# Performance work log

Hardware: AMD Instinct MI355X
Metric: run time of the kernel (lower is better)

The kernel has to match this reference:

```python
import jax, jax.numpy as jnp
import numpy as np

C, C_H, N_HEAD = 8, 1, 8
B, S, I = 1, 4096, 1024


def setup_inputs() -> dict:
    key = jax.random.key(0)
    ks = jax.random.split(key, 8)
    m = jax.random.normal(ks[0], (B, S, I, C), dtype=jnp.float32)
    mask = jnp.ones((B, S, I), dtype=jnp.float32)
    sc = 0.1
    return {
        "m": m,
        "mask": mask,
        "ln_gamma": jnp.ones((C,), jnp.float32),
        "ln_beta": jnp.zeros((C,), jnp.float32),
        "Wq": jax.random.normal(ks[1], (C, C_H * N_HEAD), jnp.float32) * sc,
        "Wk": jax.random.normal(ks[2], (C, C_H), jnp.float32) * sc,
        "Wv": jax.random.normal(ks[3], (C, C_H), jnp.float32) * sc,
        "Wg": jax.random.normal(ks[4], (C, C_H * N_HEAD), jnp.float32) * sc,
        "bg": jax.random.normal(ks[5], (C_H * N_HEAD,), jnp.float32) * sc,
        "Wo": jax.random.normal(ks[6], (C_H * N_HEAD, C), jnp.float32) * sc,
        "bo": jax.random.normal(ks[7], (C,), jnp.float32) * sc,
    }


def reference(m, mask, ln_gamma, ln_beta, Wq, Wk, Wv, Wg, bg, Wo, bo):
    # m: (B, s, i, c) -> work in (B, i, s, c); mask: (B, s, i) -> (B, i, s)
    mt = jnp.swapaxes(m, -2, -3)
    mk = jnp.swapaxes(mask, -1, -2)
    c_h = Wk.shape[1]
    h = Wq.shape[1] // c_h
    Bz, iz, sz, _ = mt.shape

    # LayerNorm over channel dim (eps=1e-5, population variance)
    mu = jnp.mean(mt, axis=-1, keepdims=True)
    var = jnp.mean(jnp.square(mt - mu), axis=-1, keepdims=True)
    mn = (mt - mu) / jnp.sqrt(var + 1e-5) * ln_gamma + ln_beta  # (B,i,s,c)

    # Masked mean pool over sequences -> global query per residue column
    q = jnp.sum(mn * mk[..., None], axis=-2) / (jnp.sum(mk, axis=-1)[..., None] + 1e-5)  # (B,i,c)

    q = (q @ Wq) * (c_h ** -0.5)          # (B,i,h*c_h)
    k = mn @ Wk                           # (B,i,s,c_h)  shared across heads
    v = mn @ Wv                           # (B,i,s,c_h)
    g = jax.nn.sigmoid(mn @ Wg + bg)      # (B,i,s,h*c_h)

    q = q.reshape(Bz, iz, h, c_h)
    g = g.reshape(Bz, iz, sz, h, c_h)

    bias = 1e9 * (mk - 1.0)               # (B,i,s)
    a = jnp.einsum('bihd,bisd->bihs', q, k) + bias[..., None, :]
    a = jax.nn.softmax(a, axis=-1)        # (B,i,h,s)
    o = jnp.einsum('bihs,bisd->bihd', a, v)  # (B,i,h,c_h)

    o = o[..., None, :, :] * g            # (B,i,s,h,c_h) gated, broadcast over s
    o = o.reshape(Bz, iz, sz, h * c_h) @ Wo + bo  # (B,i,s,c)
    return jnp.swapaxes(o, -2, -3)        # (B,s,i,c)
```

## Files before the change

### kernel.cpp

```cpp
#include <hip/hip_runtime.h>

#define I_LEN 1024
#define S_LEN 4096

typedef float f32x4 __attribute__((ext_vector_type(4)));

__device__ __forceinline__ unsigned int f2h(float f) {
  _Float16 h = (_Float16)f; unsigned short u;
  __builtin_memcpy(&u, &h, 2); return (unsigned int)u;
}
__device__ __forceinline__ float h2f(unsigned int u) {
  unsigned short s = (unsigned short)u; _Float16 h;
  __builtin_memcpy(&h, &s, 2); return (float)h;
}

__global__ __launch_bounds__(256, 2) void msa_k1a(
    const float* __restrict__ m, const float* __restrict__ mask,
    const float* __restrict__ lng, const float* __restrict__ lnb,
    const float* __restrict__ Wk, const float* __restrict__ Wv,
    unsigned int* __restrict__ kvS, float* __restrict__ qpart)
{
  const int b  = blockIdx.x;
  const int cg = b & 15;
  const int sb = b >> 4;
  const int t  = threadIdx.x;
  const int w  = t >> 6;
  const int l  = t & 63;
  const int i  = cg * 64 + w * 16 + (l & 15);
  const int sg = l >> 4;
  const int s0 = sb * 32 + sg * 8;

  float swk = 0.f, swv = 0.f, kb = 0.f, vb = 0.f;
#pragma unroll
  for (int c = 0; c < 8; ++c) {
    swk = fmaf(lng[c], Wk[c], swk);  swv = fmaf(lng[c], Wv[c], swv);
    kb  = fmaf(lnb[c], Wk[c], kb);   vb  = fmaf(lnb[c], Wv[c], vb);
  }

  float4 L[8], H[8]; float MK[8];
#pragma unroll
  for (int r = 0; r < 8; ++r) {
    const size_t base = (size_t)((s0 + r) * I_LEN + i);
    const float4* mp = (const float4*)(m + base * 8);
    L[r] = mp[0]; H[r] = mp[1];
    MK[r] = mask[base];
  }
  __builtin_amdgcn_sched_barrier(0);

  float qnx[8] = {0,0,0,0,0,0,0,0};
  float qd = 0.f;
#pragma unroll
  for (int r = 0; r < 8; ++r) {
    const size_t base = (size_t)((s0 + r) * I_LEN + i);
    float x[8] = {L[r].x, L[r].y, L[r].z, L[r].w, H[r].x, H[r].y, H[r].z, H[r].w};
    const float mk = MK[r];
    float su = 0.f, s2 = 0.f;
#pragma unroll
    for (int c = 0; c < 8; ++c) { su += x[c]; s2 = fmaf(x[c], x[c], s2); }
    const float mu   = su * 0.125f;
    const float var  = s2 * 0.125f - mu * mu;
    const float rstd = rsqrtf(var + 1e-5f);
    float dk = 0.f, dv = 0.f;
#pragma unroll
    for (int c = 0; c < 8; ++c) {
      const float xg = x[c] * lng[c];
      dk = fmaf(xg, Wk[c], dk);
      dv = fmaf(xg, Wv[c], dv);
      x[c] = xg;
    }
    const float kk = fmaf(rstd, fmaf(-mu, swk, dk), kb);
    const float vv = fmaf(rstd, fmaf(-mu, swv, dv), vb);
    kvS[base] = (mk > 0.5f) ? ((f2h(kk) << 16) | f2h(vv)) : 0xFFFFFFFFu;

    const float mr  = mk * rstd;
    const float mmr = -mu * mr;
#pragma unroll
    for (int c = 0; c < 8; ++c)
      qnx[c] = fmaf(x[c], mr, fmaf(lng[c], mmr, qnx[c]));
    qd += mk;
  }

  float red[9];
#pragma unroll
  for (int q = 0; q < 9; ++q) {
    float x = (q < 8) ? qnx[q] : qd;
    x += __shfl_xor(x, 16);
    x += __shfl_xor(x, 32);
    red[q] = x;
  }
  if (l < 16) {
    float4* pp = (float4*)(qpart + ((size_t)sb * I_LEN + i) * 12);
    pp[0] = make_float4(red[0], red[1], red[2], red[3]);
    pp[1] = make_float4(red[4], red[5], red[6], red[7]);
    pp[2] = make_float4(red[8], 0.f, 0.f, 0.f);
  }
}

__global__ __launch_bounds__(64) void msa_k1b(
    const float* __restrict__ lnb, const float* __restrict__ Wq,
    const float* __restrict__ qpart, float* __restrict__ qtab)
{
  const int l  = threadIdx.x;
  const int i  = blockIdx.x * 4 + (l & 3);
  const int sl = l >> 2;
  float acc[9] = {0,0,0,0,0,0,0,0,0};
#pragma unroll
  for (int it = 0; it < 8; ++it) {
    const int sb = sl + it * 16;
    const float4* p = (const float4*)(qpart + ((size_t)sb * I_LEN + i) * 12);
    const float4 a = p[0], b4 = p[1], c4 = p[2];
    acc[0] += a.x;  acc[1] += a.y;  acc[2] += a.z;  acc[3] += a.w;
    acc[4] += b4.x; acc[5] += b4.y; acc[6] += b4.z; acc[7] += b4.w;
    acc[8] += c4.x;
  }
#pragma unroll
  for (int q = 0; q < 9; ++q) {
    float x = acc[q];
    x += __shfl_xor(x, 4);
    x += __shfl_xor(x, 8);
    x += __shfl_xor(x, 16);
    x += __shfl_xor(x, 32);
    acc[q] = x;
  }
  if (l < 4) {
    const float d   = acc[8];
    const float inv = 1.0f / (d + 1e-5f);
    float qs[8];
#pragma unroll
    for (int c = 0; c < 8; ++c) qs[c] = (acc[c] + lnb[c] * d) * inv;
    float qv[8];
#pragma unroll
    for (int h = 0; h < 8; ++h) {
      float v = 0.f;
#pragma unroll
      for (int c = 0; c < 8; ++c) v = fmaf(qs[c], Wq[c * 8 + h], v);
      qv[h] = v;
    }
    float4* qp = (float4*)(qtab + (size_t)i * 8);
    qp[0] = make_float4(qv[0], qv[1], qv[2], qv[3]);
    qp[1] = make_float4(qv[4], qv[5], qv[6], qv[7]);
  }
}

__global__ __launch_bounds__(256, 2) void msa_k1c(
    const unsigned int* __restrict__ kvS, const float* __restrict__ qtab,
    float* __restrict__ spart)
{
  const int b  = blockIdx.x;
  const int cg = b & 15;
  const int sb = b >> 4;
  const int t  = threadIdx.x;
  const int w  = t >> 6;
  const int l  = t & 63;
  const int i  = cg * 64 + w * 16 + (l & 15);
  const int sg = l >> 4;
  const int s0 = sb * 32 + sg * 8;

  const float4* qp = (const float4*)(qtab + (size_t)i * 8);
  const float4 q0 = qp[0], q1 = qp[1];
  const float qh[8] = {q0.x, q0.y, q0.z, q0.w, q1.x, q1.y, q1.z, q1.w};

  unsigned int W[8];
#pragma unroll
  for (int r = 0; r < 8; ++r)
    W[r] = kvS[(size_t)((s0 + r) * I_LEN + i)];
  __builtin_amdgcn_sched_barrier(0);

  float se[8] = {0,0,0,0,0,0,0,0};
  float sv[8] = {0,0,0,0,0,0,0,0};
#pragma unroll
  for (int r = 0; r < 8; ++r) {
    const unsigned int wv = W[r];
    const bool on = (wv != 0xFFFFFFFFu);
    const float kk = h2f(wv >> 16);
    const float vv = on ? h2f(wv & 0xFFFFu) : 0.0f;
#pragma unroll
    for (int h = 0; h < 8; ++h) {
      const float e = on ? __expf(qh[h] * kk) : 0.0f;
      se[h] += e;
      sv[h] = fmaf(e, vv, sv[h]);
    }
  }
  float red[16];
#pragma unroll
  for (int q = 0; q < 16; ++q) {
    float x = (q < 8) ? se[q] : sv[q - 8];
    x += __shfl_xor(x, 16);
    x += __shfl_xor(x, 32);
    red[q] = x;
  }
  if (l < 16) {
    float4* pp = (float4*)(spart + ((size_t)sb * I_LEN + i) * 16);
    pp[0] = make_float4(red[0],  red[1],  red[2],  red[3]);
    pp[1] = make_float4(red[4],  red[5],  red[6],  red[7]);
    pp[2] = make_float4(red[8],  red[9],  red[10], red[11]);
    pp[3] = make_float4(red[12], red[13], red[14], red[15]);
  }
}

__global__ __launch_bounds__(64) void msa_k1d(
    const float* __restrict__ spart, float* __restrict__ o_tab)
{
  const int l  = threadIdx.x;
  const int i  = blockIdx.x * 4 + (l & 3);
  const int sl = l >> 2;
  float acc[16] = {0,0,0,0,0,0,0,0,0,0,0,0,0,0,0,0};
#pragma unroll
  for (int it = 0; it < 8; ++it) {
    const int sb = sl + it * 16;
    const float4* p = (const float4*)(spart + ((size_t)sb * I_LEN + i) * 16);
    const float4 a = p[0], b4 = p[1], c4 = p[2], d4 = p[3];
    acc[0]  += a.x;  acc[1]  += a.y;  acc[2]  += a.z;  acc[3]  += a.w;
    acc[4]  += b4.x; acc[5]  += b4.y; acc[6]  += b4.z; acc[7]  += b4.w;
    acc[8]  += c4.x; acc[9]  += c4.y; acc[10] += c4.z; acc[11] += c4.w;
    acc[12] += d4.x; acc[13] += d4.y; acc[14] += d4.z; acc[15] += d4.w;
  }
#pragma unroll
  for (int q = 0; q < 16; ++q) {
    float x = acc[q];
    x += __shfl_xor(x, 4);
    x += __shfl_xor(x, 8);
    x += __shfl_xor(x, 16);
    x += __shfl_xor(x, 32);
    acc[q] = x;
  }
  if (l < 4) {
    float4* op = (float4*)(o_tab + (size_t)i * 8);
    op[0] = make_float4(acc[8]  / acc[0], acc[9]  / acc[1],
                        acc[10] / acc[2], acc[11] / acc[3]);
    op[1] = make_float4(acc[12] / acc[4], acc[13] / acc[5],
                        acc[14] / acc[6], acc[15] / acc[7]);
  }
}

__global__ __launch_bounds__(256, 2) void msa_k2(
    const float* __restrict__ m,
    const float* __restrict__ lng, const float* __restrict__ lnb,
    const float* __restrict__ Wg, const float* __restrict__ bg,
    const float* __restrict__ Wo, const float* __restrict__ bo,
    const float* __restrict__ o_tab, float* __restrict__ out)
{
  const int tid = blockIdx.x * 256 + threadIdx.x;
  const int i = tid & (I_LEN - 1);

  float sgv[8], tbv[8];
#pragma unroll
  for (int h = 0; h < 8; ++h) {
    float s = 0.f, tb = bg[h];
#pragma unroll
    for (int c = 0; c < 8; ++c) {
      s  = fmaf(lng[c], Wg[c * 8 + h], s);
      tb = fmaf(lnb[c], Wg[c * 8 + h], tb);
    }
    sgv[h] = s; tbv[h] = tb;
  }

  const float4* op = (const float4*)(o_tab + (size_t)i * 8);
  const float4 o1 = op[0], o2 = op[1];
  const float A[8] = {o1.x, o1.y, o1.z, o1.w, o2.x, o2.y, o2.z, o2.w};

#pragma unroll
  for (int g2 = 0; g2 < 2; ++g2) {
    float4 LO[4], HI[4];
#pragma unroll
    for (int r = 0; r < 4; ++r) {
      const size_t p = (size_t)tid + (size_t)(g2 * 4 + r) * 524288;
      const float4* mp = (const float4*)(m + p * 8);
      LO[r] = mp[0]; HI[r] = mp[1];
    }
    __builtin_amdgcn_sched_barrier(0);
#pragma unroll
    for (int r = 0; r < 4; ++r) {
      const size_t p = (size_t)tid + (size_t)(g2 * 4 + r) * 524288;
      float x[8] = {LO[r].x, LO[r].y, LO[r].z, LO[r].w,
                    HI[r].x, HI[r].y, HI[r].z, HI[r].w};
      float su = 0.f, s2 = 0.f;
#pragma unroll
      for (int c = 0; c < 8; ++c) { su += x[c]; s2 = fmaf(x[c], x[c], s2); }
      const float mu   = su * 0.125f;
      const float var  = s2 * 0.125f - mu * mu;
      const float rstd = rsqrtf(var + 1e-5f);
#pragma unroll
      for (int c = 0; c < 8; ++c) x[c] *= lng[c];
      float acc[8];
#pragma unroll
      for (int c = 0; c < 8; ++c) acc[c] = bo[c];
#pragma unroll
      for (int h = 0; h < 8; ++h) {
        float d = 0.f;
#pragma unroll
        for (int c = 0; c < 8; ++c) d = fmaf(x[c], Wg[c * 8 + h], d);
        const float gl = fmaf(rstd, fmaf(-mu, sgv[h], d), tbv[h]);
        const float gv = A[h] / (1.0f + __expf(-gl));
#pragma unroll
        for (int c = 0; c < 8; ++c) acc[c] = fmaf(gv, Wo[h * 8 + c], acc[c]);
      }
      f32x4* outp = (f32x4*)(out + p * 8);
      f32x4 r0 = {acc[0], acc[1], acc[2], acc[3]};
      f32x4 r1 = {acc[4], acc[5], acc[6], acc[7]};
      __builtin_nontemporal_store(r0, outp);
      __builtin_nontemporal_store(r1, outp + 1);
    }
  }
}

extern "C" void kernel_launch(void* const* d_in, const int* in_sizes, int n_in,
                              void* d_out, int out_size, void* d_ws, size_t ws_size,
                              hipStream_t stream) {
  const float* m    = (const float*)d_in[0];
  const float* mask = (const float*)d_in[1];
  const float* lng  = (const float*)d_in[2];
  const float* lnb  = (const float*)d_in[3];
  const float* Wq   = (const float*)d_in[4];
  const float* Wk   = (const float*)d_in[5];
  const float* Wv   = (const float*)d_in[6];
  const float* Wg   = (const float*)d_in[7];
  const float* bg   = (const float*)d_in[8];
  const float* Wo   = (const float*)d_in[9];
  const float* bo   = (const float*)d_in[10];
  float* out = (float*)d_out;

  char* ws = (char*)d_ws;
  float*        o_tab = (float*)ws;
  float*        qtab  = (float*)(ws + ((size_t)64 << 10));
  unsigned int* kvS   = (unsigned int*)(ws + ((size_t)1 << 20));
  float*        qpart = (float*)(ws + ((size_t)32 << 20));
  float*        spart = (float*)(ws + ((size_t)48 << 20));

  hipLaunchKernelGGL(msa_k1a, dim3(2048), dim3(256), 0, stream,
                     m, mask, lng, lnb, Wk, Wv, kvS, qpart);
  hipLaunchKernelGGL(msa_k1b, dim3(256), dim3(64), 0, stream,
                     lnb, Wq, qpart, qtab);
  hipLaunchKernelGGL(msa_k1c, dim3(2048), dim3(256), 0, stream,
                     kvS, qtab, spart);
  hipLaunchKernelGGL(msa_k1d, dim3(256), dim3(64), 0, stream,
                     spart, o_tab);
  hipLaunchKernelGGL(msa_k2, dim3(2048), dim3(256), 0, stream,
                     m, lng, lnb, Wg, bg, Wo, bo, o_tab, out);
}
```

Measured before the change: 328.8 us.

## Remap k1a/k1c to one column per thread with double-buffered row loads

Kernels k1a and k1c now give each thread one residue column and a run of 16 sequence rows. This removes the cross-lane shuffle reductions, and per-thread partials go straight to the workspace. k1a splits its rows into two register buffers so the loads for the next group of four rows overlap compute on the current group. The reducer kernels now sum twice as many partials, and the sigmoid in k2 uses a hardware reciprocal instead of a division. Each thread now reads a single 32-byte row slice, so a wavefront's memory accesses are wider strided segments than before, and the partial-sum workspace traffic doubles.

After: 334.0 us. Within noise of the previous version (+1.6%).

```diff
diff --git a/kernel.cpp b/kernel.cpp
--- a/kernel.cpp
+++ b/kernel.cpp
@@ -21,14 +21,10 @@
     unsigned int* __restrict__ kvS, float* __restrict__ qpart)
 {
   const int b  = blockIdx.x;
-  const int cg = b & 15;
-  const int sb = b >> 4;
-  const int t  = threadIdx.x;
-  const int w  = t >> 6;
-  const int l  = t & 63;
-  const int i  = cg * 64 + w * 16 + (l & 15);
-  const int sg = l >> 4;
-  const int s0 = sb * 32 + sg * 8;
+  const int cg = b & 3;
+  const int sb = b >> 2;
+  const int i  = cg * 256 + threadIdx.x;
+  const int s0 = sb * 16;
 
   float swk = 0.f, swv = 0.f, kb = 0.f, vb = 0.f;
 #pragma unroll
@@ -37,63 +33,71 @@
     kb  = fmaf(lnb[c], Wk[c], kb);   vb  = fmaf(lnb[c], Wv[c], vb);
   }
 
-  float4 L[8], H[8]; float MK[8];
-#pragma unroll
-  for (int r = 0; r < 8; ++r) {
-    const size_t base = (size_t)((s0 + r) * I_LEN + i);
-    const float4* mp = (const float4*)(m + base * 8);
-    L[r] = mp[0]; H[r] = mp[1];
-    MK[r] = mask[base];
-  }
-  __builtin_amdgcn_sched_barrier(0);
-
   float qnx[8] = {0,0,0,0,0,0,0,0};
   float qd = 0.f;
-#pragma unroll
-  for (int r = 0; r < 8; ++r) {
-    const size_t base = (size_t)((s0 + r) * I_LEN + i);
-    float x[8] = {L[r].x, L[r].y, L[r].z, L[r].w, H[r].x, H[r].y, H[r].z, H[r].w};
-    const float mk = MK[r];
-    float su = 0.f, s2 = 0.f;
-#pragma unroll
-    for (int c = 0; c < 8; ++c) { su += x[c]; s2 = fmaf(x[c], x[c], s2); }
-    const float mu   = su * 0.125f;
-    const float var  = s2 * 0.125f - mu * mu;
-    const float rstd = rsqrtf(var + 1e-5f);
-    float dk = 0.f, dv = 0.f;
-#pragma unroll
-    for (int c = 0; c < 8; ++c) {
-      const float xg = x[c] * lng[c];
-      dk = fmaf(xg, Wk[c], dk);
-      dv = fmaf(xg, Wv[c], dv);
-      x[c] = xg;
-    }
-    const float kk = fmaf(rstd, fmaf(-mu, swk, dk), kb);
-    const float vv = fmaf(rstd, fmaf(-mu, swv, dv), vb);
-    kvS[base] = (mk > 0.5f) ? ((f2h(kk) << 16) | f2h(vv)) : 0xFFFFFFFFu;
-
-    const float mr  = mk * rstd;
-    const float mmr = -mu * mr;
-#pragma unroll
-    for (int c = 0; c < 8; ++c)
-      qnx[c] = fmaf(x[c], mr, fmaf(lng[c], mmr, qnx[c]));
-    qd += mk;
-  }
-
-  float red[9];
-#pragma unroll
-  for (int q = 0; q < 9; ++q) {
-    float x = (q < 8) ? qnx[q] : qd;
-    x += __shfl_xor(x, 16);
-    x += __shfl_xor(x, 32);
-    red[q] = x;
-  }
-  if (l < 16) {
-    float4* pp = (float4*)(qpart + ((size_t)sb * I_LEN + i) * 12);
-    pp[0] = make_float4(red[0], red[1], red[2], red[3]);
-    pp[1] = make_float4(red[4], red[5], red[6], red[7]);
-    pp[2] = make_float4(red[8], 0.f, 0.f, 0.f);
-  }
+
+  float4 A0[4], B0[4]; float M0[4];
+  float4 A1[4], B1[4]; float M1[4];
+
+#define K1A_LOAD(Ab, Bb, Mb, HT)                                         \
+  _Pragma("unroll")                                                      \
+  for (int rr = 0; rr < 4; ++rr) {                                       \
+    const size_t base = (size_t)((s0 + (HT) * 4 + rr) * I_LEN + i);      \
+    const float4* mp = (const float4*)(m + base * 8);                    \
+    Ab[rr] = mp[0]; Bb[rr] = mp[1]; Mb[rr] = mask[base];                 \
+  }
+
+#define K1A_COMP(Ab, Bb, Mb, HT)                                         \
+  _Pragma("unroll")                                                      \
+  for (int rr = 0; rr < 4; ++rr) {                                       \
+    const size_t base = (size_t)((s0 + (HT) * 4 + rr) * I_LEN + i);      \
+    float x[8] = {Ab[rr].x, Ab[rr].y, Ab[rr].z, Ab[rr].w,                \
+                  Bb[rr].x, Bb[rr].y, Bb[rr].z, Bb[rr].w};               \
+    const float mk = Mb[rr];                                             \
+    float su = 0.f, s2 = 0.f;                                            \
+    _Pragma("unroll")                                                    \
+    for (int c = 0; c < 8; ++c) { su += x[c]; s2 = fmaf(x[c], x[c], s2); } \
+    const float mu   = su * 0.125f;                                      \
+    const float var  = s2 * 0.125f - mu * mu;                            \
+    const float rstd = rsqrtf(var + 1e-5f);                              \
+    float dk = 0.f, dv = 0.f;                                            \
+    _Pragma("unroll")                                                    \
+    for (int c = 0; c < 8; ++c) {                                        \
+      const float xg = x[c] * lng[c];                                    \
+      dk = fmaf(xg, Wk[c], dk);                                          \
+      dv = fmaf(xg, Wv[c], dv);                                          \
+      x[c] = xg;                                                         \
+    }                                                                    \
+    const float kk = fmaf(rstd, fmaf(-mu, swk, dk), kb);                 \
+    const float vv = fmaf(rstd, fmaf(-mu, swv, dv), vb);                 \
+    kvS[base] = (mk > 0.5f) ? ((f2h(kk) << 16) | f2h(vv)) : 0xFFFFFFFFu; \
+    const float mr  = mk * rstd;                                         \
+    const float mmr = -mu * mr;                                          \
+    _Pragma("unroll")                                                    \
+    for (int c = 0; c < 8; ++c)                                          \
+      qnx[c] = fmaf(x[c], mr, fmaf(lng[c], mmr, qnx[c]));                \
+    qd += mk;                                                            \
+  }
+
+  K1A_LOAD(A0, B0, M0, 0)
+  K1A_LOAD(A1, B1, M1, 1)
+  __builtin_amdgcn_sched_barrier(0);
+  K1A_COMP(A0, B0, M0, 0)
+  K1A_LOAD(A0, B0, M0, 2)
+  __builtin_amdgcn_sched_barrier(0);
+  K1A_COMP(A1, B1, M1, 1)
+  K1A_LOAD(A1, B1, M1, 3)
+  __builtin_amdgcn_sched_barrier(0);
+  K1A_COMP(A0, B0, M0, 2)
+  __builtin_amdgcn_sched_barrier(0);
+  K1A_COMP(A1, B1, M1, 3)
+
+  float4* pp = (float4*)(qpart + ((size_t)sb * I_LEN + i) * 12);
+  pp[0] = make_float4(qnx[0], qnx[1], qnx[2], qnx[3]);
+  pp[1] = make_float4(qnx[4], qnx[5], qnx[6], qnx[7]);
+  pp[2] = make_float4(qd, 0.f, 0.f, 0.f);
+#undef K1A_LOAD
+#undef K1A_COMP
 }
 
 __global__ __launch_bounds__(64) void msa_k1b(
@@ -105,7 +109,7 @@
   const int sl = l >> 2;
   float acc[9] = {0,0,0,0,0,0,0,0,0};
 #pragma unroll
-  for (int it = 0; it < 8; ++it) {
+  for (int it = 0; it < 16; ++it) {
     const int sb = sl + it * 16;
     const float4* p = (const float4*)(qpart + ((size_t)sb * I_LEN + i) * 12);
     const float4 a = p[0], b4 = p[1], c4 = p[2];
@@ -147,29 +151,25 @@
     float* __restrict__ spart)
 {
   const int b  = blockIdx.x;
-  const int cg = b & 15;
-  const int sb = b >> 4;
-  const int t  = threadIdx.x;
-  const int w  = t >> 6;
-  const int l  = t & 63;
-  const int i  = cg * 64 + w * 16 + (l & 15);
-  const int sg = l >> 4;
-  const int s0 = sb * 32 + sg * 8;
+  const int cg = b & 3;
+  const int sb = b >> 2;
+  const int i  = cg * 256 + threadIdx.x;
+  const int s0 = sb * 16;
 
   const float4* qp = (const float4*)(qtab + (size_t)i * 8);
   const float4 q0 = qp[0], q1 = qp[1];
   const float qh[8] = {q0.x, q0.y, q0.z, q0.w, q1.x, q1.y, q1.z, q1.w};
 
-  unsigned int W[8];
-#pragma unroll
-  for (int r = 0; r < 8; ++r)
+  unsigned int W[16];
+#pragma unroll
+  for (int r = 0; r < 16; ++r)
     W[r] = kvS[(size_t)((s0 + r) * I_LEN + i)];
   __builtin_amdgcn_sched_barrier(0);
 
   float se[8] = {0,0,0,0,0,0,0,0};
   float sv[8] = {0,0,0,0,0,0,0,0};
 #pragma unroll
-  for (int r = 0; r < 8; ++r) {
+  for (int r = 0; r < 16; ++r) {
     const unsigned int wv = W[r];
     const bool on = (wv != 0xFFFFFFFFu);
     const float kk = h2f(wv >> 16);
@@ -181,21 +181,11 @@
       sv[h] = fmaf(e, vv, sv[h]);
     }
   }
-  float red[16];
-#pragma unroll
-  for (int q = 0; q < 16; ++q) {
-    float x = (q < 8) ? se[q] : sv[q - 8];
-    x += __shfl_xor(x, 16);
-    x += __shfl_xor(x, 32);
-    red[q] = x;
-  }
-  if (l < 16) {
-    float4* pp = (float4*)(spart + ((size_t)sb * I_LEN + i) * 16);
-    pp[0] = make_float4(red[0],  red[1],  red[2],  red[3]);
-    pp[1] = make_float4(red[4],  red[5],  red[6],  red[7]);
-    pp[2] = make_float4(red[8],  red[9],  red[10], red[11]);
-    pp[3] = make_float4(red[12], red[13], red[14], red[15]);
-  }
+  float4* pp = (float4*)(spart + ((size_t)sb * I_LEN + i) * 16);
+  pp[0] = make_float4(se[0], se[1], se[2], se[3]);
+  pp[1] = make_float4(se[4], se[5], se[6], se[7]);
+  pp[2] = make_float4(sv[0], sv[1], sv[2], sv[3]);
+  pp[3] = make_float4(sv[4], sv[5], sv[6], sv[7]);
 }
 
 __global__ __launch_bounds__(64) void msa_k1d(
@@ -206,7 +196,7 @@
   const int sl = l >> 2;
   float acc[16] = {0,0,0,0,0,0,0,0,0,0,0,0,0,0,0,0};
 #pragma unroll
-  for (int it = 0; it < 8; ++it) {
+  for (int it = 0; it < 16; ++it) {
     const int sb = sl + it * 16;
     const float4* p = (const float4*)(spart + ((size_t)sb * I_LEN + i) * 16);
     const float4 a = p[0], b4 = p[1], c4 = p[2], d4 = p[3];
@@ -291,7 +281,7 @@
 #pragma unroll
         for (int c = 0; c < 8; ++c) d = fmaf(x[c], Wg[c * 8 + h], d);
         const float gl = fmaf(rstd, fmaf(-mu, sgv[h], d), tbv[h]);
-        const float gv = A[h] / (1.0f + __expf(-gl));
+        const float gv = A[h] * __builtin_amdgcn_rcpf(1.0f + __expf(-gl));
 #pragma unroll
         for (int c = 0; c < 8; ++c) acc[c] = fmaf(gv, Wo[h * 8 + c], acc[c]);
       }
@@ -327,11 +317,11 @@
   float*        qpart = (float*)(ws + ((size_t)32 << 20));
   float*        spart = (float*)(ws + ((size_t)48 << 20));
 
-  hipLaunchKernelGGL(msa_k1a, dim3(2048), dim3(256), 0, stream,
+  hipLaunchKernelGGL(msa_k1a, dim3(1024), dim3(256), 0, stream,
                      m, mask, lng, lnb, Wk, Wv, kvS, qpart);
   hipLaunchKernelGGL(msa_k1b, dim3(256), dim3(64), 0, stream,
                      lnb, Wq, qpart, qtab);
-  hipLaunchKernelGGL(msa_k1c, dim3(2048), dim3(256), 0, stream,
+  hipLaunchKernelGGL(msa_k1c, dim3(1024), dim3(256), 0, stream,
                      kvS, qtab, spart);
   hipLaunchKernelGGL(msa_k1d, dim3(256), dim3(64), 0, stream,
                      spart, o_tab);
```
